# Kernel tuning notes

Hardware: AMD Instinct MI355X
Metric: run time of the kernel (lower is better)

The kernel has to match this reference:

```python
import jax, jax.numpy as jnp
import numpy as np

N, E, D, H = 50000, 800000, 64, 4  # nodes, edges, dim_h, heads
NEG_SLOPE = 0.2
BN_EPS = 1e-5


def setup_inputs() -> dict:
    key = jax.random.key(0)
    ks = jax.random.split(key, 8)
    x = jax.random.normal(ks[0], (N, D), dtype=jnp.float32)
    edge_index = jax.random.randint(ks[1], (2, E), 0, N, dtype=jnp.int32)
    s = 1.0 / np.sqrt(D)
    W_lin = jax.random.normal(ks[2], (D, D), dtype=jnp.float32) * s
    b_lin = jnp.zeros((D,), dtype=jnp.float32)
    prelu_w = jnp.full((D,), 0.25, dtype=jnp.float32)
    W_gat = jax.random.normal(ks[3], (H * D, D), dtype=jnp.float32) * s  # maps D -> H*D
    att_src = jax.random.normal(ks[4], (H, D), dtype=jnp.float32) * 0.1
    att_dst = jax.random.normal(ks[5], (H, D), dtype=jnp.float32) * 0.1
    gat_bias = jnp.zeros((D,), dtype=jnp.float32)
    bn_gamma = jnp.ones((D,), dtype=jnp.float32)
    bn_beta = jnp.zeros((D,), dtype=jnp.float32)
    return dict(x=x, edge_index=edge_index, W_lin=W_lin, b_lin=b_lin,
                prelu_w=prelu_w, W_gat=W_gat, att_src=att_src, att_dst=att_dst,
                gat_bias=gat_bias, bn_gamma=bn_gamma, bn_beta=bn_beta)


def _gat_mod_fwd(x, edge_index, W_lin, b_lin, prelu_w, W_gat, att_src, att_dst,
                 gat_bias, bn_gamma, bn_beta):
    # --- pre linear + PReLU ---
    x = x @ W_lin.T + b_lin
    x = jnp.where(x >= 0, x, prelu_w * x)  # per-channel PReLU

    # --- GATConv (concat=False -> head mean), add_self_loops=True ---
    h = (x @ W_gat.T).reshape(N, H, D)              # [N,H,D]
    a_src = jnp.einsum('nhd,hd->nh', h, att_src)    # [N,H]
    a_dst = jnp.einsum('nhd,hd->nh', h, att_dst)    # [N,H]

    loop = jnp.arange(N, dtype=edge_index.dtype)
    src = jnp.concatenate([edge_index[0], loop])    # [E+N]
    dst = jnp.concatenate([edge_index[1], loop])

    e = jax.nn.leaky_relu(a_src[src] + a_dst[dst], NEG_SLOPE)   # [E+N, H]
    # segment softmax over destination nodes (self loops guarantee non-empty)
    emax = jax.ops.segment_max(e, dst, num_segments=N)          # [N,H]
    p = jnp.exp(e - emax[dst])
    denom = jax.ops.segment_sum(p, dst, num_segments=N)         # [N,H]
    alpha = p / denom[dst]                                      # [E+N,H]

    msg = h[src] * alpha[:, :, None]                            # [E+N,H,D]
    out = jax.ops.segment_sum(msg, dst, num_segments=N)         # [N,H,D]
    out = out.mean(axis=1) + gat_bias                           # [N,D]

    # --- BatchNorm1d (training: batch stats) + ReLU ---
    mean = out.mean(axis=0)
    var = out.var(axis=0)
    out = bn_gamma * (out - mean) * jax.lax.rsqrt(var + BN_EPS) + bn_beta
    return jax.nn.relu(out)


def reference(x, edge_index, W_lin, b_lin, prelu_w, W_gat, att_src, att_dst,
              gat_bias, bn_gamma, bn_beta):
    return _gat_mod_fwd(x, edge_index, W_lin, b_lin, prelu_w, W_gat, att_src,
                        att_dst, gat_bias, bn_gamma, bn_beta)
```

## Files before the change

### kernel.cpp

```cpp
#include <hip/hip_runtime.h>
#include <hip/hip_fp16.h>

#define NEG_SLOPE 0.2f
#define BN_EPS 1e-5f

constexpr int D = 64;
constexpr int H = 4;

typedef _Float16 half4_t __attribute__((ext_vector_type(4)));
typedef _Float16 half8_t __attribute__((ext_vector_type(8)));
typedef float f32x4_t __attribute__((ext_vector_type(4)));
typedef int i32x4 __attribute__((ext_vector_type(4)));

union Rec {
    i32x4 i4;
    struct { int idx; int pad; half4_t w; } f;
};

#define MFMA16(a, b, c) __builtin_amdgcn_mfma_f32_16x16x32_f16(a, b, c, 0, 0, 0)

__device__ inline float lrelu(float v) { return (v >= 0.f) ? v : NEG_SLOPE * v; }

__device__ inline void split8(const float* p, bool ok, half8_t& hi, half8_t& lo) {
    float f[8];
    if (ok) {
        float4 a = *(const float4*)p;
        float4 b = *(const float4*)(p + 4);
        f[0] = a.x; f[1] = a.y; f[2] = a.z; f[3] = a.w;
        f[4] = b.x; f[5] = b.y; f[6] = b.z; f[7] = b.w;
    } else {
        #pragma unroll
        for (int j = 0; j < 8; j++) f[j] = 0.f;
    }
    #pragma unroll
    for (int j = 0; j < 8; j++) {
        _Float16 h = (_Float16)f[j];
        hi[j] = h;
        lo[j] = (_Float16)(f[j] - (float)h);
    }
}

__global__ __launch_bounds__(256) void k_node(
    const float* __restrict__ x,
    const float* __restrict__ W_lin, const float* __restrict__ b_lin,
    const float* __restrict__ prelu_w, const float* __restrict__ W_gat,
    const float* __restrict__ att_src, const float* __restrict__ att_dst,
    _Float16* __restrict__ hh, float* __restrict__ asrc_ws,
    float* __restrict__ adst_ws, const int* __restrict__ ei,
    int* __restrict__ deg8, int* __restrict__ rank, int N, int E)
{
    __shared__ _Float16 h_lds[32 * 264];
    __shared__ _Float16 x1hi[32 * 72];
    __shared__ _Float16 x1lo[32 * 72];

    const int t = threadIdx.x;
    const int w = t >> 6;
    const int l = t & 63;
    const int li = l & 15;
    const int lq = l >> 4;
    const int base = blockIdx.x * 32;
    const int nvalid = min(32, N - base);

    const int nthreads = gridDim.x * 256;
    const int e0 = blockIdx.x * 256 + t;
    const int e1 = e0 + nthreads;
    const bool v0 = e0 < E;
    const bool v1 = e1 < E;
    int r0v = 0, r1v = 0;
    {
        int d0 = 0, d1 = 0;
        if (v0) d0 = ei[E + e0];
        if (v1) d1 = ei[E + e1];
        if (v0) r0v = atomicAdd(&deg8[((e0 >> 8) & 7) * N + d0], 1);
        if (v1) r1v = atomicAdd(&deg8[((e1 >> 8) & 7) * N + d1], 1);
    }

    f32x4_t accA[2] = {};
    {
        half8_t blh[2], bll[2];
        const int n = 16 * w + li;
        #pragma unroll
        for (int ks = 0; ks < 2; ks++)
            split8(W_lin + n * 64 + 32 * ks + 8 * lq, true, blh[ks], bll[ks]);
        #pragma unroll
        for (int mt = 0; mt < 2; mt++) {
            const int row = base + 16 * mt + li;
            const bool ok = row < N;
            #pragma unroll
            for (int ks = 0; ks < 2; ks++) {
                half8_t ah, al;
                split8(x + (size_t)row * 64 + 32 * ks + 8 * lq, ok, ah, al);
                accA[mt] = MFMA16(ah, blh[ks], accA[mt]);
                accA[mt] = MFMA16(al, blh[ks], accA[mt]);
                accA[mt] = MFMA16(ah, bll[ks], accA[mt]);
            }
        }
    }

    if (v0) rank[e0] = r0v;
    if (v1) rank[e1] = r1v;

    {
        const int n = 16 * w + li;
        const float bl = b_lin[n];
        const float pw = prelu_w[n];
        #pragma unroll
        for (int mt = 0; mt < 2; mt++) {
            #pragma unroll
            for (int r = 0; r < 4; r++) {
                const int m = 16 * mt + lq * 4 + r;
                float v = accA[mt][r] + bl;
                v = (v >= 0.f) ? v : pw * v;
                _Float16 hi = (_Float16)v;
                x1hi[m * 72 + n] = hi;
                x1lo[m * 72 + n] = (_Float16)(v - (float)hi);
            }
        }
    }
    __syncthreads();

    half8_t xah[2][2], xal[2][2];
    #pragma unroll
    for (int mt = 0; mt < 2; mt++) {
        #pragma unroll
        for (int ks = 0; ks < 2; ks++) {
            const int off = (16 * mt + li) * 72 + 32 * ks + 8 * lq;
            xah[mt][ks] = *(const half8_t*)(&x1hi[off]);
            xal[mt][ks] = *(const half8_t*)(&x1lo[off]);
        }
    }
    f32x4_t accB[2][4] = {};
    #pragma unroll
    for (int nt = 0; nt < 4; nt++) {
        half8_t wh[2], wl[2];
        const int c = 64 * w + 16 * nt + li;
        #pragma unroll
        for (int ks = 0; ks < 2; ks++)
            split8(W_gat + (size_t)c * 64 + 32 * ks + 8 * lq, true, wh[ks], wl[ks]);
        #pragma unroll
        for (int mt = 0; mt < 2; mt++) {
            #pragma unroll
            for (int ks = 0; ks < 2; ks++) {
                accB[mt][nt] = MFMA16(xah[mt][ks], wh[ks], accB[mt][nt]);
                accB[mt][nt] = MFMA16(xal[mt][ks], wh[ks], accB[mt][nt]);
                accB[mt][nt] = MFMA16(xah[mt][ks], wl[ks], accB[mt][nt]);
            }
        }
    }

    {
        float asv[4], adv[4];
        #pragma unroll
        for (int nt = 0; nt < 4; nt++) {
            const int c = 64 * w + 16 * nt + li;
            asv[nt] = att_src[c];
            adv[nt] = att_dst[c];
        }
        #pragma unroll
        for (int mt = 0; mt < 2; mt++) {
            #pragma unroll
            for (int r = 0; r < 4; r++) {
                float s = 0.f, dsum = 0.f;
                #pragma unroll
                for (int nt = 0; nt < 4; nt++) {
                    s += accB[mt][nt][r] * asv[nt];
                    dsum += accB[mt][nt][r] * adv[nt];
                }
                #pragma unroll
                for (int off = 1; off < 16; off <<= 1) {
                    s += __shfl_xor(s, off, 64);
                    dsum += __shfl_xor(dsum, off, 64);
                }
                if (li == 0) {
                    const int m = 16 * mt + lq * 4 + r;
                    if (m < nvalid) {
                        asrc_ws[(size_t)(base + m) * H + w] = s;
                        adst_ws[(size_t)(base + m) * H + w] = dsum;
                    }
                }
            }
        }
    }

    #pragma unroll
    for (int mt = 0; mt < 2; mt++) {
        #pragma unroll
        for (int nt = 0; nt < 4; nt++) {
            #pragma unroll
            for (int r = 0; r < 4; r++) {
                const int m = 16 * mt + lq * 4 + r;
                const int d = 16 * nt + li;
                h_lds[m * 264 + d * 4 + w] = (_Float16)accB[mt][nt][r];
            }
        }
    }
    __syncthreads();
    {
        const int chunks = nvalid * 32;
        const uint4* src = (const uint4*)h_lds;
        uint4* dst = (uint4*)(hh + (size_t)base * 256);
        for (int i = t; i < chunks; i += 256) {
            int row = i >> 5;
            int col = i & 31;
            dst[i] = src[row * 33 + col];
        }
    }
}

__global__ __launch_bounds__(256) void k_offsets(const int* __restrict__ deg8,
                                                 int* __restrict__ pref8,
                                                 int* __restrict__ deg,
                                                 int* __restrict__ gcount,
                                                 int* __restrict__ offs, int N) {
    __shared__ int sm[256];
    __shared__ int sbase;
    int t = threadIdx.x;
    int idx = blockIdx.x * 256 + t;
    int v = 0;
    if (idx < N) {
        #pragma unroll
        for (int p = 0; p < 8; p++) {
            int c = deg8[p * N + idx];
            pref8[p * N + idx] = v;
            v += c;
        }
        deg[idx] = v;
    }
    sm[t] = v;
    __syncthreads();
    for (int off = 1; off < 256; off <<= 1) {
        int w = (t >= off) ? sm[t - off] : 0;
        __syncthreads();
        sm[t] += w;
        __syncthreads();
    }
    if (t == 255) sbase = atomicAdd(gcount, sm[255]);
    __syncthreads();
    if (idx < N) offs[idx] = sbase + sm[t] - v;
}

__global__ __launch_bounds__(256) void k_fill(const int* __restrict__ ei,
                                              const int* __restrict__ offs,
                                              const int* __restrict__ pref8,
                                              const int* __restrict__ rank,
                                              const float* __restrict__ asrc,
                                              const float* __restrict__ adst,
                                              i32x4* __restrict__ recs,
                                              int N, int E) {
    int e = blockIdx.x * 256 + threadIdx.x;
    if (e >= E) return;
    int s = ei[e];
    int d = ei[E + e];
    int p = (e >> 8) & 7;
    int r0 = rank[e];
    int pos = offs[d] + pref8[p * N + d] + r0;
    float4 a = *(const float4*)(asrc + (size_t)s * H);
    float4 b = *(const float4*)(adst + (size_t)d * H);
    Rec r;
    r.f.idx = s;
    r.f.pad = 0;
    r.f.w[0] = (_Float16)__expf(lrelu(a.x + b.x));
    r.f.w[1] = (_Float16)__expf(lrelu(a.y + b.y));
    r.f.w[2] = (_Float16)__expf(lrelu(a.z + b.z));
    r.f.w[3] = (_Float16)__expf(lrelu(a.w + b.w));
    recs[pos] = r.i4;
}

__global__ __launch_bounds__(256) void k_agg(
    const float* __restrict__ asrc, const float* __restrict__ adst,
    const int* __restrict__ offs, const int* __restrict__ deg,
    const i32x4* __restrict__ recs, const half4_t* __restrict__ hh,
    float* __restrict__ out, int N)
{
    int wid = (blockIdx.x * 256 + threadIdx.x) >> 6;
    int lane = threadIdx.x & 63;
    if (wid >= N) return;
    const int i = wid;

    float4 b = *(const float4*)(adst + (size_t)i * H);
    float4 a0 = *(const float4*)(asrc + (size_t)i * H);
    float ws0 = __expf(lrelu(a0.x + b.x));
    float ws1 = __expf(lrelu(a0.y + b.y));
    float ws2 = __expf(lrelu(a0.z + b.z));
    float ws3 = __expf(lrelu(a0.w + b.w));

    const int beg = offs[i];
    const int dg = deg[i];

    float den0 = ws0, den1 = ws1, den2 = ws2, den3 = ws3;
    float acc0, acc1, acc2, acc3;
    {
        half4_t hv = hh[(size_t)i * D + lane];
        acc0 = ws0 * (float)hv[0];
        acc1 = ws1 * (float)hv[1];
        acc2 = ws2 * (float)hv[2];
        acc3 = ws3 * (float)hv[3];
    }
    int k = 0;
    for (; k + 4 <= dg; k += 4) {
        Rec r0, r1, r2, r3;
        r0.i4 = recs[beg + k];
        r1.i4 = recs[beg + k + 1];
        r2.i4 = recs[beg + k + 2];
        r3.i4 = recs[beg + k + 3];
        half4_t h0 = hh[(size_t)r0.f.idx * D + lane];
        half4_t h1 = hh[(size_t)r1.f.idx * D + lane];
        half4_t h2 = hh[(size_t)r2.f.idx * D + lane];
        half4_t h3 = hh[(size_t)r3.f.idx * D + lane];
        float w00 = (float)r0.f.w[0], w01 = (float)r0.f.w[1],
              w02 = (float)r0.f.w[2], w03 = (float)r0.f.w[3];
        float w10 = (float)r1.f.w[0], w11 = (float)r1.f.w[1],
              w12 = (float)r1.f.w[2], w13 = (float)r1.f.w[3];
        float w20 = (float)r2.f.w[0], w21 = (float)r2.f.w[1],
              w22 = (float)r2.f.w[2], w23 = (float)r2.f.w[3];
        float w30 = (float)r3.f.w[0], w31 = (float)r3.f.w[1],
              w32 = (float)r3.f.w[2], w33 = (float)r3.f.w[3];
        den0 += w00 + w10 + w20 + w30;
        den1 += w01 + w11 + w21 + w31;
        den2 += w02 + w12 + w22 + w32;
        den3 += w03 + w13 + w23 + w33;
        acc0 += w00 * (float)h0[0] + w10 * (float)h1[0] +
                w20 * (float)h2[0] + w30 * (float)h3[0];
        acc1 += w01 * (float)h0[1] + w11 * (float)h1[1] +
                w21 * (float)h2[1] + w31 * (float)h3[1];
        acc2 += w02 * (float)h0[2] + w12 * (float)h1[2] +
                w22 * (float)h2[2] + w32 * (float)h3[2];
        acc3 += w03 * (float)h0[3] + w13 * (float)h1[3] +
                w23 * (float)h2[3] + w33 * (float)h3[3];
    }
    for (; k < dg; k++) {
        Rec r;
        r.i4 = recs[beg + k];
        half4_t hv = hh[(size_t)r.f.idx * D + lane];
        float w0 = (float)r.f.w[0], w1 = (float)r.f.w[1];
        float w2 = (float)r.f.w[2], w3 = (float)r.f.w[3];
        den0 += w0; den1 += w1; den2 += w2; den3 += w3;
        acc0 += w0 * (float)hv[0];
        acc1 += w1 * (float)hv[1];
        acc2 += w2 * (float)hv[2];
        acc3 += w3 * (float)hv[3];
    }

    out[(size_t)i * D + lane] =
        0.25f * (acc0 / den0 + acc1 / den1 + acc2 / den2 + acc3 / den3);
}

__global__ __launch_bounds__(256) void k_bn_stats(const float* __restrict__ out,
                                                  float* __restrict__ sums,
                                                  int total) {
    const int t = threadIdx.x;
    const int stride = gridDim.x * 256;
    float s = 0.f, sq = 0.f;
    for (int idx = blockIdx.x * 256 + t; idx < total; idx += stride) {
        float v = out[idx];
        s += v;
        sq += v * v;
    }
    __shared__ float ls[256], lq[256];
    ls[t] = s;
    lq[t] = sq;
    __syncthreads();
    if (t < 64) {
        s = ls[t] + ls[t + 64] + ls[t + 128] + ls[t + 192];
        sq = lq[t] + lq[t + 64] + lq[t + 128] + lq[t + 192];
        atomicAdd(&sums[t], s);
        atomicAdd(&sums[64 + t], sq);
    }
}

__global__ __launch_bounds__(256) void k_bn_apply(float* __restrict__ out,
                                                  const float* __restrict__ sums,
                                                  const float* __restrict__ gamma,
                                                  const float* __restrict__ beta,
                                                  int total, float invN) {
    int idx = blockIdx.x * 256 + threadIdx.x;
    if (idx >= total) return;
    int c = idx & 63;
    float mean = sums[c] * invN;
    float var = sums[64 + c] * invN - mean * mean;
    float y = gamma[c] * (out[idx] - mean) * rsqrtf(var + BN_EPS) + beta[c];
    out[idx] = fmaxf(y, 0.f);
}

extern "C" void kernel_launch(void* const* d_in, const int* in_sizes, int n_in,
                              void* d_out, int out_size, void* d_ws, size_t ws_size,
                              hipStream_t stream) {
    const float* x       = (const float*)d_in[0];
    const int*   ei      = (const int*)d_in[1];
    const float* W_lin   = (const float*)d_in[2];
    const float* b_lin   = (const float*)d_in[3];
    const float* prelu_w = (const float*)d_in[4];
    const float* W_gat   = (const float*)d_in[5];
    const float* att_src = (const float*)d_in[6];
    const float* att_dst = (const float*)d_in[7];
    const float* bn_gamma = (const float*)d_in[9];
    const float* bn_beta  = (const float*)d_in[10];
    float* out = (float*)d_out;

    const int N = in_sizes[0] / D;
    const int E = in_sizes[1] / 2;

    char* wp = (char*)d_ws;
    _Float16* hh = (_Float16*)wp;      wp += (size_t)N * D * H * sizeof(_Float16);
    float* asrc  = (float*)wp;          wp += (size_t)N * H * sizeof(float);
    float* adst  = (float*)wp;          wp += (size_t)N * H * sizeof(float);
    char* zero_base = wp;
    float* sums  = (float*)wp;          wp += 2 * D * sizeof(float);
    int* deg8    = (int*)wp;            wp += (size_t)8 * N * sizeof(int);
    int* gcount  = (int*)wp;            wp += 4 * sizeof(int);
    size_t zero_bytes = (size_t)(wp - zero_base);
    int* pref8   = (int*)wp;            wp += (size_t)8 * N * sizeof(int);
    int* deg     = (int*)wp;            wp += (size_t)N * sizeof(int);
    int* offs    = (int*)wp;            wp += (size_t)N * sizeof(int);
    int* rank    = (int*)wp;            wp += (size_t)E * sizeof(int);
    i32x4* recs  = (i32x4*)wp;          wp += ((size_t)E + 4) * sizeof(i32x4);
    (void)ws_size; (void)n_in; (void)out_size;

    const int total = N * D;
    const int NB = (N + 255) / 256;

    hipMemsetAsync(zero_base, 0, zero_bytes, stream);
    hipLaunchKernelGGL(k_node, dim3((N + 31) / 32), dim3(256), 0, stream,
                       x, W_lin, b_lin, prelu_w, W_gat, att_src, att_dst,
                       hh, asrc, adst, ei, deg8, rank, N, E);
    hipLaunchKernelGGL(k_offsets, dim3(NB), dim3(256), 0, stream,
                       deg8, pref8, deg, gcount, offs, N);
    hipLaunchKernelGGL(k_fill, dim3((E + 255) / 256), dim3(256), 0, stream,
                       ei, offs, pref8, rank, asrc, adst, recs, N, E);
    hipLaunchKernelGGL(k_agg, dim3((N + 3) / 4), dim3(256), 0, stream,
                       asrc, adst, offs, deg, recs, (const half4_t*)hh, out, N);
    hipLaunchKernelGGL(k_bn_stats, dim3(1024), dim3(256), 0, stream,
                       out, sums, total);
    hipLaunchKernelGGL(k_bn_apply, dim3((total + 255) / 256), dim3(256), 0, stream,
                       out, sums, bn_gamma, bn_beta, total, 1.f / (float)N);
}
```

Baseline: 265.8 us.

## Fuse BN statistics into aggregation and use packed fp16 dot products

The aggregation kernel now gathers 8 edges per iteration and pairs edges so that v_dot2 (fdot2) instructions accumulate the weighted fp16 features and denominators. The edge-count tail goes through one padded 8-wide pass with zeroed weights. The batch-norm sum and sum-of-squares are accumulated directly in the aggregation kernel through atomics spread over 8 partial buffers, which removes the separate stats kernel and its full reread of the output. The cost is heavy atomic traffic, one pair of atomics per node per lane, plus fp16 accumulation inside dot2 and extra wasted gathers on the padded tail.

```diff
diff --git a/kernel.cpp b/kernel.cpp
--- a/kernel.cpp
+++ b/kernel.cpp
@@ -7,6 +7,7 @@
 constexpr int D = 64;
 constexpr int H = 4;
 
+typedef _Float16 half2_t __attribute__((ext_vector_type(2)));
 typedef _Float16 half4_t __attribute__((ext_vector_type(4)));
 typedef _Float16 half8_t __attribute__((ext_vector_type(8)));
 typedef float f32x4_t __attribute__((ext_vector_type(4)));
@@ -18,6 +19,14 @@
 };
 
 #define MFMA16(a, b, c) __builtin_amdgcn_mfma_f32_16x16x32_f16(a, b, c, 0, 0, 0)
+
+#if __has_builtin(__builtin_amdgcn_fdot2)
+#define FDOT2(a, b, c) __builtin_amdgcn_fdot2((a), (b), (c), false)
+#else
+#define FDOT2(a, b, c) ((c) + (float)(a)[0] * (float)(b)[0] + (float)(a)[1] * (float)(b)[1])
+#endif
+
+__device__ inline half2_t h2cast(unsigned int u) { return __builtin_bit_cast(half2_t, u); }
 
 __device__ inline float lrelu(float v) { return (v >= 0.f) ? v : NEG_SLOPE * v; }
 
@@ -266,11 +275,35 @@
     recs[pos] = r.i4;
 }
 
+__device__ inline void edge_pair(const i32x4 ra, const i32x4 rb,
+                                 const uint2 ha, const uint2 hb,
+                                 float& den0, float& den1, float& den2, float& den3,
+                                 float& acc0, float& acc1, float& acc2, float& acc3)
+{
+    const half2_t one2 = h2cast(0x3C003C00u);
+    unsigned int wp0 = __builtin_amdgcn_perm((unsigned int)rb.z, (unsigned int)ra.z, 0x05040100u);
+    unsigned int wp1 = __builtin_amdgcn_perm((unsigned int)rb.z, (unsigned int)ra.z, 0x07060302u);
+    unsigned int wp2 = __builtin_amdgcn_perm((unsigned int)rb.w, (unsigned int)ra.w, 0x05040100u);
+    unsigned int wp3 = __builtin_amdgcn_perm((unsigned int)rb.w, (unsigned int)ra.w, 0x07060302u);
+    unsigned int hp0 = __builtin_amdgcn_perm(hb.x, ha.x, 0x05040100u);
+    unsigned int hp1 = __builtin_amdgcn_perm(hb.x, ha.x, 0x07060302u);
+    unsigned int hp2 = __builtin_amdgcn_perm(hb.y, ha.y, 0x05040100u);
+    unsigned int hp3 = __builtin_amdgcn_perm(hb.y, ha.y, 0x07060302u);
+    den0 = FDOT2(h2cast(wp0), one2, den0);
+    den1 = FDOT2(h2cast(wp1), one2, den1);
+    den2 = FDOT2(h2cast(wp2), one2, den2);
+    den3 = FDOT2(h2cast(wp3), one2, den3);
+    acc0 = FDOT2(h2cast(wp0), h2cast(hp0), acc0);
+    acc1 = FDOT2(h2cast(wp1), h2cast(hp1), acc1);
+    acc2 = FDOT2(h2cast(wp2), h2cast(hp2), acc2);
+    acc3 = FDOT2(h2cast(wp3), h2cast(hp3), acc3);
+}
+
 __global__ __launch_bounds__(256) void k_agg(
     const float* __restrict__ asrc, const float* __restrict__ adst,
     const int* __restrict__ offs, const int* __restrict__ deg,
-    const i32x4* __restrict__ recs, const half4_t* __restrict__ hh,
-    float* __restrict__ out, int N)
+    const i32x4* __restrict__ recs, const uint2* __restrict__ hh2,
+    float* __restrict__ out, float* __restrict__ sums8, int N)
 {
     int wid = (blockIdx.x * 256 + threadIdx.x) >> 6;
     int lane = threadIdx.x & 63;
@@ -284,100 +317,79 @@
     float ws2 = __expf(lrelu(a0.z + b.z));
     float ws3 = __expf(lrelu(a0.w + b.w));
 
-    const int beg = offs[i];
-    const int dg = deg[i];
+    const int beg = __builtin_amdgcn_readfirstlane(offs[i]);
+    const int dg  = __builtin_amdgcn_readfirstlane(deg[i]);
 
     float den0 = ws0, den1 = ws1, den2 = ws2, den3 = ws3;
     float acc0, acc1, acc2, acc3;
     {
-        half4_t hv = hh[(size_t)i * D + lane];
-        acc0 = ws0 * (float)hv[0];
-        acc1 = ws1 * (float)hv[1];
-        acc2 = ws2 * (float)hv[2];
-        acc3 = ws3 * (float)hv[3];
-    }
+        uint2 hv = hh2[(size_t)i * D + lane];
+        half2_t s01 = h2cast(hv.x), s23 = h2cast(hv.y);
+        acc0 = ws0 * (float)s01[0];
+        acc1 = ws1 * (float)s01[1];
+        acc2 = ws2 * (float)s23[0];
+        acc3 = ws3 * (float)s23[1];
+    }
+
+    const int nfull = dg & ~7;
     int k = 0;
-    for (; k + 4 <= dg; k += 4) {
-        Rec r0, r1, r2, r3;
-        r0.i4 = recs[beg + k];
-        r1.i4 = recs[beg + k + 1];
-        r2.i4 = recs[beg + k + 2];
-        r3.i4 = recs[beg + k + 3];
-        half4_t h0 = hh[(size_t)r0.f.idx * D + lane];
-        half4_t h1 = hh[(size_t)r1.f.idx * D + lane];
-        half4_t h2 = hh[(size_t)r2.f.idx * D + lane];
-        half4_t h3 = hh[(size_t)r3.f.idx * D + lane];
-        float w00 = (float)r0.f.w[0], w01 = (float)r0.f.w[1],
-              w02 = (float)r0.f.w[2], w03 = (float)r0.f.w[3];
-        float w10 = (float)r1.f.w[0], w11 = (float)r1.f.w[1],
-              w12 = (float)r1.f.w[2], w13 = (float)r1.f.w[3];
-        float w20 = (float)r2.f.w[0], w21 = (float)r2.f.w[1],
-              w22 = (float)r2.f.w[2], w23 = (float)r2.f.w[3];
-        float w30 = (float)r3.f.w[0], w31 = (float)r3.f.w[1],
-              w32 = (float)r3.f.w[2], w33 = (float)r3.f.w[3];
-        den0 += w00 + w10 + w20 + w30;
-        den1 += w01 + w11 + w21 + w31;
-        den2 += w02 + w12 + w22 + w32;
-        den3 += w03 + w13 + w23 + w33;
-        acc0 += w00 * (float)h0[0] + w10 * (float)h1[0] +
-                w20 * (float)h2[0] + w30 * (float)h3[0];
-        acc1 += w01 * (float)h0[1] + w11 * (float)h1[1] +
-                w21 * (float)h2[1] + w31 * (float)h3[1];
-        acc2 += w02 * (float)h0[2] + w12 * (float)h1[2] +
-                w22 * (float)h2[2] + w32 * (float)h3[2];
-        acc3 += w03 * (float)h0[3] + w13 * (float)h1[3] +
-                w23 * (float)h2[3] + w33 * (float)h3[3];
-    }
-    for (; k < dg; k++) {
-        Rec r;
-        r.i4 = recs[beg + k];
-        half4_t hv = hh[(size_t)r.f.idx * D + lane];
-        float w0 = (float)r.f.w[0], w1 = (float)r.f.w[1];
-        float w2 = (float)r.f.w[2], w3 = (float)r.f.w[3];
-        den0 += w0; den1 += w1; den2 += w2; den3 += w3;
-        acc0 += w0 * (float)hv[0];
-        acc1 += w1 * (float)hv[1];
-        acc2 += w2 * (float)hv[2];
-        acc3 += w3 * (float)hv[3];
-    }
-
-    out[(size_t)i * D + lane] =
-        0.25f * (acc0 / den0 + acc1 / den1 + acc2 / den2 + acc3 / den3);
-}
-
-__global__ __launch_bounds__(256) void k_bn_stats(const float* __restrict__ out,
-                                                  float* __restrict__ sums,
-                                                  int total) {
-    const int t = threadIdx.x;
-    const int stride = gridDim.x * 256;
-    float s = 0.f, sq = 0.f;
-    for (int idx = blockIdx.x * 256 + t; idx < total; idx += stride) {
-        float v = out[idx];
-        s += v;
-        sq += v * v;
-    }
-    __shared__ float ls[256], lq[256];
-    ls[t] = s;
-    lq[t] = sq;
-    __syncthreads();
-    if (t < 64) {
-        s = ls[t] + ls[t + 64] + ls[t + 128] + ls[t + 192];
-        sq = lq[t] + lq[t + 64] + lq[t + 128] + lq[t + 192];
-        atomicAdd(&sums[t], s);
-        atomicAdd(&sums[64 + t], sq);
-    }
+    for (; k < nfull; k += 8) {
+        i32x4 rr[8];
+        #pragma unroll
+        for (int j = 0; j < 8; j++)
+            rr[j] = __builtin_nontemporal_load(recs + beg + k + j);
+        uint2 hv[8];
+        #pragma unroll
+        for (int j = 0; j < 8; j++)
+            hv[j] = hh2[(size_t)rr[j].x * D + lane];
+        #pragma unroll
+        for (int j = 0; j < 8; j += 2)
+            edge_pair(rr[j], rr[j + 1], hv[j], hv[j + 1],
+                      den0, den1, den2, den3, acc0, acc1, acc2, acc3);
+    }
+    if (k < dg) {
+        i32x4 rr[8];
+        #pragma unroll
+        for (int j = 0; j < 8; j++) {
+            int kk = min(k + j, dg - 1);
+            i32x4 r = __builtin_nontemporal_load(recs + beg + kk);
+            if (k + j >= dg) { r.z = 0; r.w = 0; }
+            rr[j] = r;
+        }
+        uint2 hv[8];
+        #pragma unroll
+        for (int j = 0; j < 8; j++)
+            hv[j] = hh2[(size_t)rr[j].x * D + lane];
+        #pragma unroll
+        for (int j = 0; j < 8; j += 2)
+            edge_pair(rr[j], rr[j + 1], hv[j], hv[j + 1],
+                      den0, den1, den2, den3, acc0, acc1, acc2, acc3);
+    }
+
+    float v = 0.25f * (acc0 / den0 + acc1 / den1 + acc2 / den2 + acc3 / den3);
+    out[(size_t)i * D + lane] = v;
+
+    int p = wid & 7;
+    atomicAdd(&sums8[p * 128 + lane], v);
+    atomicAdd(&sums8[p * 128 + 64 + lane], v * v);
 }
 
 __global__ __launch_bounds__(256) void k_bn_apply(float* __restrict__ out,
-                                                  const float* __restrict__ sums,
+                                                  const float* __restrict__ sums8,
                                                   const float* __restrict__ gamma,
                                                   const float* __restrict__ beta,
                                                   int total, float invN) {
     int idx = blockIdx.x * 256 + threadIdx.x;
     if (idx >= total) return;
     int c = idx & 63;
-    float mean = sums[c] * invN;
-    float var = sums[64 + c] * invN - mean * mean;
+    float s = 0.f, q = 0.f;
+    #pragma unroll
+    for (int p = 0; p < 8; p++) {
+        s += sums8[p * 128 + c];
+        q += sums8[p * 128 + 64 + c];
+    }
+    float mean = s * invN;
+    float var = q * invN - mean * mean;
     float y = gamma[c] * (out[idx] - mean) * rsqrtf(var + BN_EPS) + beta[c];
     out[idx] = fmaxf(y, 0.f);
 }
@@ -405,7 +417,7 @@
     float* asrc  = (float*)wp;          wp += (size_t)N * H * sizeof(float);
     float* adst  = (float*)wp;          wp += (size_t)N * H * sizeof(float);
     char* zero_base = wp;
-    float* sums  = (float*)wp;          wp += 2 * D * sizeof(float);
+    float* sums8 = (float*)wp;          wp += (size_t)8 * 128 * sizeof(float);
     int* deg8    = (int*)wp;            wp += (size_t)8 * N * sizeof(int);
     int* gcount  = (int*)wp;            wp += 4 * sizeof(int);
     size_t zero_bytes = (size_t)(wp - zero_base);
@@ -428,9 +440,7 @@
     hipLaunchKernelGGL(k_fill, dim3((E + 255) / 256), dim3(256), 0, stream,
                        ei, offs, pref8, rank, asrc, adst, recs, N, E);
     hipLaunchKernelGGL(k_agg, dim3((N + 3) / 4), dim3(256), 0, stream,
-                       asrc, adst, offs, deg, recs, (const half4_t*)hh, out, N);
-    hipLaunchKernelGGL(k_bn_stats, dim3(1024), dim3(256), 0, stream,
-                       out, sums, total);
+                       asrc, adst, offs, deg, recs, (const uint2*)hh, out, sums8, N);
     hipLaunchKernelGGL(k_bn_apply, dim3((total + 255) / 256), dim3(256), 0, stream,
-                       out, sums, bn_gamma, bn_beta, total, 1.f / (float)N);
-}
+                       out, sums8, bn_gamma, bn_beta, total, 1.f / (float)N);
+}
```

Result: slower. 344.5 us (+29.6%).
